# Kernel tuning notes

Hardware: AMD Instinct MI355X
Metric: run time of the kernel (lower is better)

Reference implementation:

```python
import jax, jax.numpy as jnp
import numpy as np

KERNEL_SIZES = (3, 7, 15, 31)


def setup_inputs() -> dict:
    key = jax.random.key(0)
    x = jax.random.normal(key, (16, 4096, 512), dtype=jnp.float32)
    kernel_weights = jnp.ones((len(KERNEL_SIZES),), dtype=jnp.float32) / len(KERNEL_SIZES)
    return {"x": x, "kernel_weights": kernel_weights}


def _box_avg(xc, k):
    # xc: [B, F, S] channels-first; replicate-pad then depthwise box filter of width k
    B, Fc, S = xc.shape
    p = k // 2
    xp = jnp.pad(xc, ((0, 0), (0, 0), (p, p)), mode='edge')
    kern = jnp.full((Fc, 1, k), 1.0 / k, dtype=xc.dtype)  # depthwise: O=F, I/groups=1
    return jax.lax.conv_general_dilated(
        xp, kern, window_strides=(1,), padding='VALID',
        dimension_numbers=('NCW', 'OIW', 'NCW'), feature_group_count=Fc)


def reference(x, kernel_weights):
    # x: [B, S, F]
    w = jax.nn.softmax(kernel_weights)  # softmax over the 4 scales
    xc = jnp.transpose(x, (0, 2, 1))    # [B, F, S]
    out = jnp.zeros_like(xc)
    for i, k in enumerate(KERNEL_SIZES):
        out = out + w[i] * _box_avg(xc, k)
    return jnp.transpose(out, (0, 2, 1))  # [B, S, F]
```

## Files before the change

kernel.cpp:

```cpp
#include <hip/hip_runtime.h>
#include <math.h>

constexpr int B = 16;
constexpr int S = 4096;
constexpr int F = 512;
constexpr int L = 64;
constexpr int BLOCK = 256;

__global__ __launch_bounds__(BLOCK) void msavg_kernel(
    const float* __restrict__ x, const float* __restrict__ kw,
    float* __restrict__ out) {
  const int f  = blockIdx.x * BLOCK + threadIdx.x;
  const int t0 = blockIdx.y * L;
  const int b  = blockIdx.z;

  float w0 = kw[0], w1 = kw[1], w2 = kw[2], w3 = kw[3];
  float m  = fmaxf(fmaxf(w0, w1), fmaxf(w2, w3));
  float e0 = expf(w0 - m), e1 = expf(w1 - m), e2 = expf(w2 - m), e3 = expf(w3 - m);
  float inv = 1.0f / (e0 + e1 + e2 + e3);
  const float c3  = e0 * inv * (1.0f / 3.0f);
  const float c7  = e1 * inv * (1.0f / 7.0f);
  const float c15 = e2 * inv * (1.0f / 15.0f);
  const float c31 = e3 * inv * (1.0f / 31.0f);

  const float* xb = x   + ((size_t)b * S) * F + f;
  float*       ob = out + ((size_t)b * S) * F + f;

  float prev[32], cur[32];

  {
    float p = 0.0f;
#pragma unroll
    for (int j = 0; j < 32; ++j) {
      int s = t0 - 16 + j;
      s = s < 0 ? 0 : (s > S - 1 ? S - 1 : s);
      p += xb[(size_t)s * F];
      prev[j] = p;
    }
  }

#pragma unroll
  for (int g = 0; g < L / 32; ++g) {
    const int T = t0 + g * 32;

    float xv[32];
    if (T + 47 <= S - 1) {
#pragma unroll
      for (int j = 0; j < 32; ++j) xv[j] = xb[(size_t)(T + 16 + j) * F];
    } else {
#pragma unroll
      for (int j = 0; j < 32; ++j) {
        int s = T + 16 + j;
        s = s > S - 1 ? S - 1 : s;
        xv[j] = xb[(size_t)s * F];
      }
    }

    {
      float p = prev[31];
#pragma unroll
      for (int j = 0; j < 32; ++j) {
        p += xv[j];
        cur[j] = p;
      }
    }

#pragma unroll
    for (int j = 0; j < 32; ++j) {
      float Pp15 = (j < 1)  ? prev[j + 31] : cur[j - 1];
      float Pp7  = (j < 9)  ? prev[j + 23] : cur[j - 9];
      float Pp3  = (j < 13) ? prev[j + 19] : cur[j - 13];
      float Pp1  = (j < 15) ? prev[j + 17] : cur[j - 15];
      float Pm2  = (j < 18) ? prev[j + 14] : cur[j - 18];
      float Pm4  = (j < 20) ? prev[j + 12] : cur[j - 20];
      float Pm8  = (j < 24) ? prev[j + 8]  : cur[j - 24];
      float Pm16 = prev[j];
      float o = c3  * (Pp1  - Pm2) +
                c7  * (Pp3  - Pm4) +
                c15 * (Pp7  - Pm8) +
                c31 * (Pp15 - Pm16);
      ob[(size_t)(T + j) * F] = o;
    }

#pragma unroll
    for (int j = 0; j < 32; ++j) prev[j] = cur[j];
  }
}

extern "C" void kernel_launch(void* const* d_in, const int* in_sizes, int n_in,
                              void* d_out, int out_size, void* d_ws, size_t ws_size,
                              hipStream_t stream) {
  const float* x  = (const float*)d_in[0];
  const float* kw = (const float*)d_in[1];
  float* out = (float*)d_out;
  (void)in_sizes; (void)n_in; (void)out_size; (void)d_ws; (void)ws_size;

  dim3 grid(F / BLOCK, S / L, B);
  msavg_kernel<<<grid, BLOCK, 0, stream>>>(x, kw, out);
}
```

Baseline: 239.0 us.

## Load full 96-row window up front with sched barrier and nontemporal stores

Replaces the two-phase prev/cur pipelined loads with a single batch of 96 loads per thread into one register array, fenced by a sched_barrier so every load issues before any compute. It then runs one prefix sum and computes all 64 outputs from it, writing them with nontemporal stores. Launch bounds now request 4 blocks per SM. The aim is more memory-level parallelism and less cache pollution from the output, at the cost of higher register pressure from the 96-element array.

```diff
diff --git a/kernel.cpp b/kernel.cpp
--- a/kernel.cpp
+++ b/kernel.cpp
@@ -5,9 +5,11 @@
 constexpr int S = 4096;
 constexpr int F = 512;
 constexpr int L = 64;
+constexpr int HALO = 16;
+constexpr int NV = L + 2 * HALO;
 constexpr int BLOCK = 256;
 
-__global__ __launch_bounds__(BLOCK) void msavg_kernel(
+__global__ __launch_bounds__(BLOCK, 4) void msavg_kernel(
     const float* __restrict__ x, const float* __restrict__ kw,
     float* __restrict__ out) {
   const int f  = blockIdx.x * BLOCK + threadIdx.x;
@@ -26,64 +28,34 @@
   const float* xb = x   + ((size_t)b * S) * F + f;
   float*       ob = out + ((size_t)b * S) * F + f;
 
-  float prev[32], cur[32];
+  float v[NV];
+  if (t0 - HALO >= 0 && t0 + L - 1 + HALO <= S - 1) {
+    const float* p0 = xb + (size_t)(t0 - HALO) * F;
+#pragma unroll
+    for (int j = 0; j < NV; ++j) v[j] = p0[(size_t)j * F];
+  } else {
+#pragma unroll
+    for (int j = 0; j < NV; ++j) {
+      int s = t0 - HALO + j;
+      s = s < 0 ? 0 : (s > S - 1 ? S - 1 : s);
+      v[j] = xb[(size_t)s * F];
+    }
+  }
+  __builtin_amdgcn_sched_barrier(0);
 
   {
     float p = 0.0f;
 #pragma unroll
-    for (int j = 0; j < 32; ++j) {
-      int s = t0 - 16 + j;
-      s = s < 0 ? 0 : (s > S - 1 ? S - 1 : s);
-      p += xb[(size_t)s * F];
-      prev[j] = p;
-    }
+    for (int j = 0; j < NV; ++j) { p += v[j]; v[j] = p; }
   }
 
 #pragma unroll
-  for (int g = 0; g < L / 32; ++g) {
-    const int T = t0 + g * 32;
-
-    float xv[32];
-    if (T + 47 <= S - 1) {
-#pragma unroll
-      for (int j = 0; j < 32; ++j) xv[j] = xb[(size_t)(T + 16 + j) * F];
-    } else {
-#pragma unroll
-      for (int j = 0; j < 32; ++j) {
-        int s = T + 16 + j;
-        s = s > S - 1 ? S - 1 : s;
-        xv[j] = xb[(size_t)s * F];
-      }
-    }
-
-    {
-      float p = prev[31];
-#pragma unroll
-      for (int j = 0; j < 32; ++j) {
-        p += xv[j];
-        cur[j] = p;
-      }
-    }
-
-#pragma unroll
-    for (int j = 0; j < 32; ++j) {
-      float Pp15 = (j < 1)  ? prev[j + 31] : cur[j - 1];
-      float Pp7  = (j < 9)  ? prev[j + 23] : cur[j - 9];
-      float Pp3  = (j < 13) ? prev[j + 19] : cur[j - 13];
-      float Pp1  = (j < 15) ? prev[j + 17] : cur[j - 15];
-      float Pm2  = (j < 18) ? prev[j + 14] : cur[j - 18];
-      float Pm4  = (j < 20) ? prev[j + 12] : cur[j - 20];
-      float Pm8  = (j < 24) ? prev[j + 8]  : cur[j - 24];
-      float Pm16 = prev[j];
-      float o = c3  * (Pp1  - Pm2) +
-                c7  * (Pp3  - Pm4) +
-                c15 * (Pp7  - Pm8) +
-                c31 * (Pp15 - Pm16);
-      ob[(size_t)(T + j) * F] = o;
-    }
-
-#pragma unroll
-    for (int j = 0; j < 32; ++j) prev[j] = cur[j];
+  for (int i = 0; i < L; ++i) {
+    float o = c3  * (v[i + 17] - v[i + 14]) +
+              c7  * (v[i + 19] - v[i + 12]) +
+              c15 * (v[i + 23] - v[i + 8 ]) +
+              c31 * (v[i + 31] - v[i     ]);
+    __builtin_nontemporal_store(o, &ob[(size_t)(t0 + i) * F]);
   }
 }
 
```

New measurement: 313.0 us. +31.0%, slower.

## Software-pipeline loads of next chunk and lengthen per-block time span

Applied to the files above, without the earlier changes.

Each block now processes 128 time steps in four 32-step chunks instead of 64 steps, and prefetches the next chunk's inputs into registers before computing the current one, with sched barriers to keep the loads issued early. Initial halo loads are issued together without clamping on interior blocks, and the prefix sum is computed after the loads instead of interleaved with them. This aims to hide global-memory latency and cut halo re-reads, at the cost of more registers and fewer blocks.

```diff
diff --git a/kernel.cpp b/kernel.cpp
--- a/kernel.cpp
+++ b/kernel.cpp
@@ -4,14 +4,15 @@
 constexpr int B = 16;
 constexpr int S = 4096;
 constexpr int F = 512;
-constexpr int L = 64;
+constexpr int L = 32;
+constexpr int CH = 4;
 constexpr int BLOCK = 256;
 
 __global__ __launch_bounds__(BLOCK) void msavg_kernel(
     const float* __restrict__ x, const float* __restrict__ kw,
     float* __restrict__ out) {
   const int f  = blockIdx.x * BLOCK + threadIdx.x;
-  const int t0 = blockIdx.y * L;
+  const int t0 = blockIdx.y * (CH * L);
   const int b  = blockIdx.z;
 
   float w0 = kw[0], w1 = kw[1], w2 = kw[2], w3 = kw[3];
@@ -26,54 +27,72 @@
   const float* xb = x   + ((size_t)b * S) * F + f;
   float*       ob = out + ((size_t)b * S) * F + f;
 
-  float prev[32], cur[32];
+  const bool ledge = (blockIdx.y == 0);
+  const bool redge = (blockIdx.y == gridDim.y - 1);
+
+  float prev[32], xv[32], xn[32];
+
+  if (ledge) {
+#pragma unroll
+    for (int i = 0; i < 32; ++i) {
+      int s = t0 - 16 + i;
+      s = s < 0 ? 0 : s;
+      prev[i] = xb[(size_t)s * F];
+    }
+  } else {
+    const float* p0 = xb + (size_t)(t0 - 16) * F;
+#pragma unroll
+    for (int i = 0; i < 32; ++i) prev[i] = p0[(size_t)i * F];
+  }
+  {
+    const float* p1 = xb + (size_t)(t0 + 16) * F;
+#pragma unroll
+    for (int j = 0; j < 32; ++j) xv[j] = p1[(size_t)j * F];
+  }
+  __builtin_amdgcn_sched_barrier(0);
 
   {
     float p = 0.0f;
 #pragma unroll
-    for (int j = 0; j < 32; ++j) {
-      int s = t0 - 16 + j;
-      s = s < 0 ? 0 : (s > S - 1 ? S - 1 : s);
-      p += xb[(size_t)s * F];
-      prev[j] = p;
-    }
+    for (int i = 0; i < 32; ++i) { p += prev[i]; prev[i] = p; }
   }
 
 #pragma unroll
-  for (int g = 0; g < L / 32; ++g) {
-    const int T = t0 + g * 32;
+  for (int c = 0; c < CH; ++c) {
+    const int T = t0 + c * L;
 
-    float xv[32];
-    if (T + 47 <= S - 1) {
+    if (c + 1 < CH) {
+      const int sn = T + 48;
+      if (redge && sn + 31 > S - 1) {
 #pragma unroll
-      for (int j = 0; j < 32; ++j) xv[j] = xb[(size_t)(T + 16 + j) * F];
-    } else {
+        for (int j = 0; j < 32; ++j) {
+          int s = sn + j;
+          s = s > S - 1 ? S - 1 : s;
+          xn[j] = xb[(size_t)s * F];
+        }
+      } else {
+        const float* pn = xb + (size_t)sn * F;
 #pragma unroll
-      for (int j = 0; j < 32; ++j) {
-        int s = T + 16 + j;
-        s = s > S - 1 ? S - 1 : s;
-        xv[j] = xb[(size_t)s * F];
+        for (int j = 0; j < 32; ++j) xn[j] = pn[(size_t)j * F];
       }
+      __builtin_amdgcn_sched_barrier(0);
     }
 
     {
       float p = prev[31];
 #pragma unroll
-      for (int j = 0; j < 32; ++j) {
-        p += xv[j];
-        cur[j] = p;
-      }
+      for (int j = 0; j < 32; ++j) { p += xv[j]; xv[j] = p; }
     }
 
 #pragma unroll
-    for (int j = 0; j < 32; ++j) {
-      float Pp15 = (j < 1)  ? prev[j + 31] : cur[j - 1];
-      float Pp7  = (j < 9)  ? prev[j + 23] : cur[j - 9];
-      float Pp3  = (j < 13) ? prev[j + 19] : cur[j - 13];
-      float Pp1  = (j < 15) ? prev[j + 17] : cur[j - 15];
-      float Pm2  = (j < 18) ? prev[j + 14] : cur[j - 18];
-      float Pm4  = (j < 20) ? prev[j + 12] : cur[j - 20];
-      float Pm8  = (j < 24) ? prev[j + 8]  : cur[j - 24];
+    for (int j = 0; j < L; ++j) {
+      float Pp15 = (j < 1)  ? prev[j + 31] : xv[j - 1];
+      float Pp7  = (j < 9)  ? prev[j + 23] : xv[j - 9];
+      float Pp3  = (j < 13) ? prev[j + 19] : xv[j - 13];
+      float Pp1  = (j < 15) ? prev[j + 17] : xv[j - 15];
+      float Pm2  = (j < 18) ? prev[j + 14] : xv[j - 18];
+      float Pm4  = (j < 20) ? prev[j + 12] : xv[j - 20];
+      float Pm8  = (j < 24) ? prev[j + 8]  : xv[j - 24];
       float Pm16 = prev[j];
       float o = c3  * (Pp1  - Pm2) +
                 c7  * (Pp3  - Pm4) +
@@ -82,8 +101,10 @@
       ob[(size_t)(T + j) * F] = o;
     }
 
+    if (c + 1 < CH) {
 #pragma unroll
-    for (int j = 0; j < 32; ++j) prev[j] = cur[j];
+      for (int j = 0; j < 32; ++j) { prev[j] = xv[j]; xv[j] = xn[j]; }
+    }
   }
 }
 
@@ -95,6 +116,6 @@
   float* out = (float*)d_out;
   (void)in_sizes; (void)n_in; (void)out_size; (void)d_ws; (void)ws_size;
 
-  dim3 grid(F / BLOCK, S / L, B);
+  dim3 grid(F / BLOCK, S / (CH * L), B);
   msavg_kernel<<<grid, BLOCK, 0, stream>>>(x, kw, out);
 }
```

New measurement: 238.2 us. No clear change (-0.3%).

## Stage input rows through LDS with async global_load_lds double buffering

Applied to the files above, without the earlier changes.

The kernel now handles 128 sequence rows by the full 512 features in each 512-thread block. Input rows are staged into a double-buffered LDS tile using global_load_lds DMA, replacing per-thread strided global loads. The prefix-sum window slides in 16-row chunks, and the loads for the next tile are issued before compute on the current one. This cuts the halo overfetch ratio and should overlap memory latency with compute. The cost is a vmcnt(0) wait plus a block barrier every chunk, and the tile occupies 64KB of LDS.

```diff
diff --git a/kernel.cpp b/kernel.cpp
--- a/kernel.cpp
+++ b/kernel.cpp
@@ -4,15 +4,45 @@
 constexpr int B = 16;
 constexpr int S = 4096;
 constexpr int F = 512;
-constexpr int L = 64;
-constexpr int BLOCK = 256;
+
+constexpr int BLOCK  = 512;
+constexpr int RPB    = 128;
+constexpr int CHUNK  = 16;
+constexpr int NCHUNK = RPB / CHUNK;
+constexpr int TROWS  = 16;
+constexpr int NTILE  = (RPB + 32) / TROWS;
+constexpr int TILE_FLOATS = TROWS * F;
+constexpr int SBLK   = S / RPB;
+
+
+__device__ __forceinline__ void gld_lds16(const float* g, float* l) {
+  __builtin_amdgcn_global_load_lds(
+      (const __attribute__((address_space(1))) void*)g,
+      (__attribute__((address_space(3))) void*)l, 16, 0, 0);
+}
+
+__device__ __forceinline__ void stage_tile(const float* xb, float* lbase,
+                                           int rbase, int wav, int lane) {
+#pragma unroll
+  for (int i = 0; i < 4; ++i) {
+    const int h = wav * 4 + i;
+    int r = rbase + (h >> 1);
+    r = r < 0 ? 0 : (r > S - 1 ? S - 1 : r);
+    const float* g = xb + (size_t)r * F + (h & 1) * 256 + lane * 4;
+    gld_lds16(g, lbase + h * 256);
+  }
+}
 
 __global__ __launch_bounds__(BLOCK) void msavg_kernel(
     const float* __restrict__ x, const float* __restrict__ kw,
     float* __restrict__ out) {
-  const int f  = blockIdx.x * BLOCK + threadIdx.x;
-  const int t0 = blockIdx.y * L;
-  const int b  = blockIdx.z;
+  __shared__ float smem[2 * TILE_FLOATS];
+
+  const int tid  = threadIdx.x;
+  const int wav  = tid >> 6;
+  const int lane = tid & 63;
+  const int r0   = blockIdx.x * RPB;
+  const int b    = blockIdx.y;
 
   float w0 = kw[0], w1 = kw[1], w2 = kw[2], w3 = kw[3];
   float m  = fmaxf(fmaxf(w0, w1), fmaxf(w2, w3));
@@ -23,67 +53,74 @@
   const float c15 = e2 * inv * (1.0f / 15.0f);
   const float c31 = e3 * inv * (1.0f / 31.0f);
 
-  const float* xb = x   + ((size_t)b * S) * F + f;
-  float*       ob = out + ((size_t)b * S) * F + f;
+  const float* xb = x   + (size_t)b * S * F;
+  float*       ob = out + (size_t)b * S * F + tid;
 
-  float prev[32], cur[32];
+  stage_tile(xb, smem,               r0 - 16, wav, lane);
+  stage_tile(xb, smem + TILE_FLOATS, r0,      wav, lane);
+  __builtin_amdgcn_sched_barrier(0);
+  asm volatile("s_waitcnt vmcnt(0)" ::: "memory");
+  __builtin_amdgcn_s_barrier();
+  __builtin_amdgcn_sched_barrier(0);
 
+  float prev[32];
   {
     float p = 0.0f;
 #pragma unroll
     for (int j = 0; j < 32; ++j) {
-      int s = t0 - 16 + j;
-      s = s < 0 ? 0 : (s > S - 1 ? S - 1 : s);
-      p += xb[(size_t)s * F];
+      p += smem[(j >> 4) * TILE_FLOATS + (j & 15) * F + tid];
       prev[j] = p;
     }
   }
+  __builtin_amdgcn_sched_barrier(0);
+  __builtin_amdgcn_s_barrier();
+  __builtin_amdgcn_sched_barrier(0);
+
+  stage_tile(xb, smem, r0 + 16, wav, lane);
+  __builtin_amdgcn_sched_barrier(0);
+  asm volatile("s_waitcnt vmcnt(0)" ::: "memory");
+  __builtin_amdgcn_s_barrier();
+  __builtin_amdgcn_sched_barrier(0);
 
 #pragma unroll
-  for (int g = 0; g < L / 32; ++g) {
-    const int T = t0 + g * 32;
+  for (int c = 0; c < NCHUNK; ++c) {
+    if (c + 3 < NTILE)
+      stage_tile(xb, smem + ((c + 3) & 1) * TILE_FLOATS,
+                 r0 - 16 + (c + 3) * TROWS, wav, lane);
 
-    float xv[32];
-    if (T + 47 <= S - 1) {
-#pragma unroll
-      for (int j = 0; j < 32; ++j) xv[j] = xb[(size_t)(T + 16 + j) * F];
-    } else {
-#pragma unroll
-      for (int j = 0; j < 32; ++j) {
-        int s = T + 16 + j;
-        s = s > S - 1 ? S - 1 : s;
-        xv[j] = xb[(size_t)s * F];
-      }
-    }
-
+    const float* tb = smem + (c & 1) * TILE_FLOATS;
+    float cur[CHUNK];
     {
       float p = prev[31];
 #pragma unroll
-      for (int j = 0; j < 32; ++j) {
-        p += xv[j];
+      for (int j = 0; j < CHUNK; ++j) {
+        p += tb[j * F + tid];
         cur[j] = p;
       }
     }
 
+    const int T = r0 + c * CHUNK;
 #pragma unroll
-    for (int j = 0; j < 32; ++j) {
-      float Pp15 = (j < 1)  ? prev[j + 31] : cur[j - 1];
+    for (int j = 0; j < CHUNK; ++j) {
+      float Pp1  = (j < 15) ? prev[j + 17] : cur[j - 15];
+      float Pp3  = (j < 13) ? prev[j + 19] : cur[j - 13];
       float Pp7  = (j < 9)  ? prev[j + 23] : cur[j - 9];
-      float Pp3  = (j < 13) ? prev[j + 19] : cur[j - 13];
-      float Pp1  = (j < 15) ? prev[j + 17] : cur[j - 15];
-      float Pm2  = (j < 18) ? prev[j + 14] : cur[j - 18];
-      float Pm4  = (j < 20) ? prev[j + 12] : cur[j - 20];
-      float Pm8  = (j < 24) ? prev[j + 8]  : cur[j - 24];
-      float Pm16 = prev[j];
-      float o = c3  * (Pp1  - Pm2) +
-                c7  * (Pp3  - Pm4) +
-                c15 * (Pp7  - Pm8) +
-                c31 * (Pp15 - Pm16);
+      float Pp15 = (j < 1)  ? prev[31]     : cur[j - 1];
+      float o = c3  * (Pp1  - prev[j + 14]) +
+                c7  * (Pp3  - prev[j + 12]) +
+                c15 * (Pp7  - prev[j + 8 ]) +
+                c31 * (Pp15 - prev[j]);
       ob[(size_t)(T + j) * F] = o;
     }
 
 #pragma unroll
-    for (int j = 0; j < 32; ++j) prev[j] = cur[j];
+    for (int i = 0; i < 32; ++i)
+      prev[i] = (i < CHUNK) ? prev[i + CHUNK] : cur[i - CHUNK];
+
+    __builtin_amdgcn_sched_barrier(0);
+    asm volatile("s_waitcnt vmcnt(0)" ::: "memory");
+    __builtin_amdgcn_s_barrier();
+    __builtin_amdgcn_sched_barrier(0);
   }
 }
 
@@ -95,6 +132,6 @@
   float* out = (float*)d_out;
   (void)in_sizes; (void)n_in; (void)out_size; (void)d_ws; (void)ws_size;
 
-  dim3 grid(F / BLOCK, S / L, B);
+  dim3 grid(SBLK, B);
   msavg_kernel<<<grid, BLOCK, 0, stream>>>(x, kw, out);
 }
```

Measured after the change: 239.1 us. No clear change (+0.1%).
